# Performance work log

Hardware: AMD Instinct MI355X
Metric: run time of the kernel (lower is better)

Reference implementation:

```python
import jax, jax.numpy as jnp
import numpy as np

T = 4096
C = 2048
N_FEAT = 2048
NEG = -1e30  # finite stand-in for -inf so fully-masked (padding) rows stay NaN-free


def setup_inputs() -> dict:
    key = jax.random.key(0)
    kx, kw, kb = jax.random.split(key, 3)
    x = jax.random.normal(kx, (T, C), dtype=jnp.float32)
    # Dense(features=3*n_feat): kernel (C, 3*n_feat), bias (3*n_feat,)
    W = jax.random.normal(kw, (C, 3 * N_FEAT), dtype=jnp.float32) * (1.0 / np.sqrt(C))
    b = jax.random.normal(kb, (3 * N_FEAT,), dtype=jnp.float32) * 0.01
    n_padd = 128
    return {"x": x, "W": W, "b": b, "n_padd": n_padd}


def reference(x, W, b, n_padd):
    T_, _ = x.shape
    qkv = x @ W + b                      # (T, 3*n_feat)
    q, k, v = jnp.split(qkv, 3, axis=1)  # each (T, n_feat)
    scale = 1.0 / jnp.sqrt(jnp.float32(q.shape[1]))
    att = (q @ k.T) * scale              # (T, T)
    rows = jnp.arange(T_)[:, None]
    cols = jnp.arange(T_)[None, :]
    # causal AND both row/col past the left padding
    mask = (cols <= rows) & (cols >= n_padd) & (rows >= n_padd)
    att = jnp.where(mask, att, NEG)
    p = jax.nn.softmax(att, axis=1)      # stable row softmax
    # kernel only stores rows >= n_padd; padding rows are zero
    p = jnp.where(rows >= n_padd, p, 0.0)
    y = p @ v                            # (T, n_feat)
    return y
```

## Files before the change

kernel.cpp:

```cpp
#include <hip/hip_runtime.h>
#include <cstdint>


#define T_DIM 4096
#define C_DIM 2048
#define NF    2048
#define N3    6144
#define NEGV  (-1e30f)

typedef __bf16 bf16x8 __attribute__((ext_vector_type(8)));
typedef __bf16 bf16x4 __attribute__((ext_vector_type(4)));
typedef float  f32x4  __attribute__((ext_vector_type(4)));

__device__ __forceinline__ void async_cp16(const void* g, void* l) {
    __builtin_amdgcn_global_load_lds(
        reinterpret_cast<const __attribute__((address_space(1))) unsigned int*>(
            reinterpret_cast<uintptr_t>(g)),
        reinterpret_cast<__attribute__((address_space(3))) unsigned int*>(
            reinterpret_cast<uintptr_t>(l)),
        16, 0, 0);
}

__device__ __forceinline__ void gemm_loop(const __bf16* A, const __bf16* B,
                                          int lda, int ldb, int m0, int n0,
                                          int kiters, __bf16* As, __bf16* Bs,
                                          f32x4 (&acc)[4][4]) {
    const int t    = threadIdx.x;
    const int wv   = t >> 6;
    const int lane = t & 63;
    const int srow = t >> 3;
    const int scol = (((t & 7) ^ (srow & 7)) << 3);
    const int wm   = (wv >> 1) << 6;
    const int wn   = (wv & 1) << 6;
    const int lrow = lane & 15;
    const int kq   = lane >> 4;
    const int swz  = lrow & 7;
    const int rc0  = ((kq ^ swz) << 3);
    const int rc1  = (((kq | 4) ^ swz) << 3);

    const __bf16* ga = A + (size_t)(m0 + srow) * lda + scol;
    const __bf16* gb = B + (size_t)(n0 + srow) * ldb + scol;

    for (int kk = 0; kk < kiters; ++kk) {
#pragma unroll
        for (int i = 0; i < 4; ++i) {
            async_cp16(ga + (size_t)(32 * i) * lda, &As[i * 2048 + wv * 512]);
            async_cp16(gb + (size_t)(32 * i) * ldb, &Bs[i * 2048 + wv * 512]);
        }
        ga += 64; gb += 64;
        __syncthreads();

#pragma unroll
        for (int kb = 0; kb < 2; ++kb) {
            const int rc = kb ? rc1 : rc0;
            bf16x8 af[4], bfr[4];
#pragma unroll
            for (int mi = 0; mi < 4; ++mi)
                af[mi] = *(const bf16x8*)&As[(wm + mi * 16 + lrow) * 64 + rc];
#pragma unroll
            for (int ni = 0; ni < 4; ++ni)
                bfr[ni] = *(const bf16x8*)&Bs[(wn + ni * 16 + lrow) * 64 + rc];
#pragma unroll
            for (int mi = 0; mi < 4; ++mi)
#pragma unroll
                for (int ni = 0; ni < 4; ++ni)
                    acc[mi][ni] = __builtin_amdgcn_mfma_f32_16x16x32_bf16(
                        af[mi], bfr[ni], acc[mi][ni], 0, 0, 0);
        }
        __syncthreads();
    }
}

__global__ void prep_kernel(const float* __restrict__ x,
                            __bf16* __restrict__ xb,
                            const float* __restrict__ W,
                            __bf16* __restrict__ Wt) {
    if (blockIdx.x < 2048) {
        const int n4 = (T_DIM * C_DIM) / 4;
        const int stride = 2048 * 256;
        for (int i = blockIdx.x * 256 + threadIdx.x; i < n4; i += stride) {
            float4 v = ((const float4*)x)[i];
            bf16x4 o;
            o[0] = (__bf16)v.x; o[1] = (__bf16)v.y;
            o[2] = (__bf16)v.z; o[3] = (__bf16)v.w;
            ((bf16x4*)xb)[i] = o;
        }
        return;
    }
    __shared__ float tile[32][33];
    const int tb = blockIdx.x - 2048;
    const int bx = (tb % (N3 / 32)) * 32;
    const int by = (tb / (N3 / 32)) * 32;
    const int tx = threadIdx.x & 31, ty = threadIdx.x >> 5;
#pragma unroll
    for (int i = 0; i < 32; i += 8)
        tile[ty + i][tx] = W[(size_t)(by + ty + i) * N3 + bx + tx];
    __syncthreads();
#pragma unroll
    for (int i = 0; i < 32; i += 8)
        Wt[(size_t)(bx + ty + i) * C_DIM + by + tx] = (__bf16)tile[tx][ty + i];
}

#define EPILOG_SETUP()                                     \
    const int t = threadIdx.x, wv = t >> 6, lane = t & 63; \
    const int wm = (wv >> 1) << 6, wn = (wv & 1) << 6;     \
    const int rq = (lane >> 4) << 2, cn = lane & 15

__global__ void __launch_bounds__(512)
qkv_gemm_kernel(const __bf16* __restrict__ xb, const __bf16* __restrict__ Wt,
                const float* __restrict__ bias, __bf16* __restrict__ qb,
                __bf16* __restrict__ kb, __bf16* __restrict__ vT) {
    __shared__ __bf16 As[3][256 * 64];
    __shared__ __bf16 Bs[3][128 * 64];

    const int t    = threadIdx.x;
    const int wv   = t >> 6;
    const int lane = t & 63;
    const int srow = t >> 3;
    const int scol = (((t & 7) ^ (srow & 7)) << 3);
    const int m0   = blockIdx.x * 256;
    const int n0   = blockIdx.y * 128;
    const int wmo  = (wv >> 1) << 6;
    const int wno  = (wv & 1) << 6;
    const int lrow = lane & 15;
    const int kq   = lane >> 4;
    const int swz  = lrow & 7;
    const int rc0  = ((kq ^ swz) << 3);
    const int rc1  = (((kq | 4) ^ swz) << 3);

    const __bf16* ga = xb + (size_t)(m0 + srow) * C_DIM + scol;
    const __bf16* gb = Wt + (size_t)(n0 + srow) * C_DIM + scol;

    f32x4 acc[4][4] = {};

    auto stage = [&](int kt, int s) {
        const __bf16* a  = ga + kt * 64;
        const __bf16* b2 = gb + kt * 64;
#pragma unroll
        for (int i = 0; i < 4; ++i)
            async_cp16(a + (size_t)(64 * i) * C_DIM, &As[s][i * 4096 + wv * 512]);
#pragma unroll
        for (int i = 0; i < 2; ++i)
            async_cp16(b2 + (size_t)(64 * i) * C_DIM, &Bs[s][i * 4096 + wv * 512]);
    };

    auto compute = [&](int s) {
        const __bf16* Ab = As[s];
        const __bf16* Bb = Bs[s];
        bf16x8 af[4][2], bfr[4][2];
#pragma unroll
        for (int mi = 0; mi < 4; ++mi) {
            const __bf16* r = &Ab[(wmo + mi * 16 + lrow) * 64];
            af[mi][0] = *(const bf16x8*)&r[rc0];
            af[mi][1] = *(const bf16x8*)&r[rc1];
        }
#pragma unroll
        for (int ni = 0; ni < 4; ++ni) {
            const __bf16* r = &Bb[(wno + ni * 16 + lrow) * 64];
            bfr[ni][0] = *(const bf16x8*)&r[rc0];
            bfr[ni][1] = *(const bf16x8*)&r[rc1];
        }
        __builtin_amdgcn_s_setprio(1);
#pragma unroll
        for (int kh = 0; kh < 2; ++kh)
#pragma unroll
            for (int mi = 0; mi < 4; ++mi)
#pragma unroll
                for (int ni = 0; ni < 4; ++ni)
                    acc[mi][ni] = __builtin_amdgcn_mfma_f32_16x16x32_bf16(
                        af[mi][kh], bfr[ni][kh], acc[mi][ni], 0, 0, 0);
        __builtin_amdgcn_s_setprio(0);
    };

    constexpr int KT = C_DIM / 64;
    stage(0, 0);
    stage(1, 1);

    int s0 = 0, s1 = 1, s2 = 2;
    for (int kt = 0; kt < KT - 2; ++kt) {
        asm volatile("s_waitcnt vmcnt(6)" ::: "memory");
        __builtin_amdgcn_s_barrier();
        asm volatile("" ::: "memory");
        stage(kt + 2, s2);
        compute(s0);
        int tmp = s0; s0 = s1; s1 = s2; s2 = tmp;
    }
    asm volatile("s_waitcnt vmcnt(6)" ::: "memory");
    __builtin_amdgcn_s_barrier();
    asm volatile("" ::: "memory");
    compute(s0);
    { int tmp = s0; s0 = s1; s1 = s2; s2 = tmp; }
    asm volatile("s_waitcnt vmcnt(0)" ::: "memory");
    __builtin_amdgcn_s_barrier();
    asm volatile("" ::: "memory");
    compute(s0);

    const int rq = (lane >> 4) << 2, cn = lane & 15;
    if (n0 >= 2 * NF) {
#pragma unroll
        for (int mi = 0; mi < 4; ++mi)
#pragma unroll
            for (int ni = 0; ni < 4; ++ni) {
                int col = n0 + wno + ni * 16 + cn;
                float bv = bias[col];
                bf16x4 o;
#pragma unroll
                for (int r = 0; r < 4; ++r) o[r] = (__bf16)(acc[mi][ni][r] + bv);
                int row = m0 + wmo + mi * 16 + rq;
                *(bf16x4*)&vT[(size_t)(col - 2 * NF) * T_DIM + row] = o;
            }
    } else {
#pragma unroll
        for (int mi = 0; mi < 4; ++mi)
#pragma unroll
            for (int ni = 0; ni < 4; ++ni) {
                int col = n0 + wno + ni * 16 + cn;
                float bv = bias[col];
#pragma unroll
                for (int r = 0; r < 4; ++r) {
                    int row = m0 + wmo + mi * 16 + rq + r;
                    float val = acc[mi][ni][r] + bv;
                    if (col < NF)
                        qb[(size_t)row * NF + col] = (__bf16)val;
                    else
                        kb[(size_t)row * NF + (col - NF)] = (__bf16)val;
                }
            }
    }
}

__global__ void __launch_bounds__(256)
sc_gemm_kernel(const __bf16* __restrict__ qb, const __bf16* __restrict__ kb,
               __bf16* __restrict__ S, const int* __restrict__ npadd_p) {
    int i = blockIdx.x;
    int mt = (int)((sqrtf(8.0f * (float)i + 1.0f) - 1.0f) * 0.5f);
    while ((mt + 1) * (mt + 2) / 2 <= i) ++mt;
    while (mt * (mt + 1) / 2 > i) --mt;
    int nt = i - mt * (mt + 1) / 2;
    const int m0 = mt * 128, n0 = nt * 128;
    const int npadd = *npadd_p;
    if (m0 + 128 <= npadd || n0 + 128 <= npadd) return;

    __shared__ __bf16 As[128 * 64];
    __shared__ __bf16 Bs[128 * 64];
    f32x4 acc[4][4] = {};
    gemm_loop(qb, kb, NF, NF, m0, n0, NF / 64, As, Bs, acc);

    const float scale = 0.022097086912079608f;
    EPILOG_SETUP();
#pragma unroll
    for (int mi = 0; mi < 4; ++mi)
#pragma unroll
        for (int ni = 0; ni < 4; ++ni) {
            int j = n0 + wn + ni * 16 + cn;
#pragma unroll
            for (int r = 0; r < 4; ++r) {
                int row = m0 + wm + mi * 16 + rq + r;
                S[(size_t)row * T_DIM + j] = (__bf16)(acc[mi][ni][r] * scale);
            }
        }
}

__global__ void __launch_bounds__(256)
softmax_kernel(const __bf16* __restrict__ S, __bf16* __restrict__ P,
               const int* __restrict__ npadd_p) {
    const int wv = threadIdx.x >> 6, lane = threadIdx.x & 63;
    const int row = blockIdx.x * 4 + wv;
    const int npadd = *npadd_p;
    __bf16* prow = P + (size_t)row * T_DIM;

    if (row < npadd) {
        bf16x8 z = {};
#pragma unroll
        for (int c = 0; c < 8; ++c) ((bf16x8*)prow)[c * 64 + lane] = z;
        return;
    }

    const __bf16* srow = S + (size_t)row * T_DIM;
    float vals[64];
    float mx = NEGV;
#pragma unroll
    for (int c = 0; c < 8; ++c) {
        if (c * 512 > row) {
#pragma unroll
            for (int e = 0; e < 8; ++e) vals[c * 8 + e] = NEGV;
            continue;
        }
        int j0 = c * 512 + lane * 8;
        bf16x8 v = ((const bf16x8*)srow)[c * 64 + lane];
#pragma unroll
        for (int e = 0; e < 8; ++e) {
            float f = (j0 + e >= npadd && j0 + e <= row) ? (float)v[e] : NEGV;
            vals[c * 8 + e] = f;
            mx = fmaxf(mx, f);
        }
    }
#pragma unroll
    for (int o = 32; o > 0; o >>= 1) mx = fmaxf(mx, __shfl_xor(mx, o));

    float sm = 0.f;
#pragma unroll
    for (int k = 0; k < 64; ++k) {
        vals[k] = exp2f((vals[k] - mx) * 1.4426950408889634f);
        sm += vals[k];
    }
#pragma unroll
    for (int o = 32; o > 0; o >>= 1) sm += __shfl_xor(sm, o);
    float inv = 1.0f / sm;

#pragma unroll
    for (int c = 0; c < 8; ++c) {
        bf16x8 o;
#pragma unroll
        for (int e = 0; e < 8; ++e) o[e] = (__bf16)(vals[c * 8 + e] * inv);
        ((bf16x8*)prow)[c * 64 + lane] = o;
    }
}

__global__ void __launch_bounds__(256)
pv_gemm_kernel(const __bf16* __restrict__ P, const __bf16* __restrict__ vT,
               float* __restrict__ out, const int* __restrict__ npadd_p) {
    const int idx = blockIdx.x;
    const int kskip = *npadd_p >> 6;
    int mt, nt, start, iters;
    bool atomic_out;
    if (idx < 256) {
        mt = idx & 15; nt = idx >> 4;
        int kt = (mt + 1) * 2 - kskip; if (kt < 0) kt = 0;
        start = kskip; iters = kt; atomic_out = false;
    } else {
        int j = idx - 256;
        mt = 16 + (j & 15); nt = (j >> 4) & 15;
        int half = j >> 8;
        int kt = (mt + 1) * 2 - kskip; if (kt < 0) kt = 0;
        int h0 = (kt + 1) >> 1;
        start = kskip + (half ? h0 : 0);
        iters = half ? kt - h0 : h0;
        atomic_out = true;
    }
    const int m0 = mt * 128, n0 = nt * 128;

    __shared__ __bf16 As[128 * 64];
    __shared__ __bf16 Bs[128 * 64];
    f32x4 acc[4][4] = {};
    gemm_loop(P + (size_t)start * 64, vT + (size_t)start * 64,
              T_DIM, T_DIM, m0, n0, iters, As, Bs, acc);

    EPILOG_SETUP();
#pragma unroll
    for (int mi = 0; mi < 4; ++mi)
#pragma unroll
        for (int ni = 0; ni < 4; ++ni) {
            int col = n0 + wn + ni * 16 + cn;
#pragma unroll
            for (int r = 0; r < 4; ++r) {
                int row = m0 + wm + mi * 16 + rq + r;
                float* p = &out[(size_t)row * NF + col];
                if (atomic_out) unsafeAtomicAdd(p, acc[mi][ni][r]);
                else            *p = acc[mi][ni][r];
            }
        }
}

extern "C" void kernel_launch(void* const* d_in, const int* in_sizes, int n_in,
                              void* d_out, int out_size, void* d_ws,
                              size_t ws_size, hipStream_t stream) {
    const float* x = (const float*)d_in[0];
    const float* W = (const float*)d_in[1];
    const float* b = (const float*)d_in[2];
    const int* npadd = (const int*)d_in[3];
    float* out = (float*)d_out;

    char* ws = (char*)d_ws;
    __bf16* xb = (__bf16*)(ws);
    __bf16* Wt = (__bf16*)(ws + (16ull << 20));
    __bf16* qb = (__bf16*)(ws + (40ull << 20));
    __bf16* kb = (__bf16*)(ws + (56ull << 20));
    __bf16* vT = (__bf16*)(ws + (72ull << 20));
    __bf16* S  = (__bf16*)(ws + (88ull << 20));
    __bf16* P  = (__bf16*)(ws + (40ull << 20));

    hipMemsetAsync(out + (size_t)2048 * NF, 0, (size_t)2048 * NF * 4, stream);

    prep_kernel<<<2048 + (N3 / 32) * (C_DIM / 32), 256, 0, stream>>>(x, xb, W, Wt);
    qkv_gemm_kernel<<<dim3(T_DIM / 256, N3 / 128), 512, 0, stream>>>(xb, Wt, b,
                                                                     qb, kb, vT);
    sc_gemm_kernel<<<528, 256, 0, stream>>>(qb, kb, S, npadd);
    softmax_kernel<<<T_DIM / 4, 256, 0, stream>>>(S, P, npadd);
    pv_gemm_kernel<<<768, 256, 0, stream>>>(P, vT, out, npadd);
}
```

Measured before the change: 335.4 us.

## Double-buffer shared GEMM loop and enlarge QKV GEMM tile to 256x384

```diff
diff --git a/kernel.cpp b/kernel.cpp
--- a/kernel.cpp
+++ b/kernel.cpp
@@ -25,6 +25,7 @@
                                           int lda, int ldb, int m0, int n0,
                                           int kiters, __bf16* As, __bf16* Bs,
                                           f32x4 (&acc)[4][4]) {
+    if (kiters <= 0) return;
     const int t    = threadIdx.x;
     const int wv   = t >> 6;
     const int lane = t & 63;
@@ -41,33 +42,51 @@
     const __bf16* ga = A + (size_t)(m0 + srow) * lda + scol;
     const __bf16* gb = B + (size_t)(n0 + srow) * ldb + scol;
 
+    auto stage = [&](int kk, int s) {
+#pragma unroll
+        for (int i = 0; i < 4; ++i) {
+            async_cp16(ga + kk * 64 + (size_t)(32 * i) * lda,
+                       &As[s * 8192 + i * 2048 + wv * 512]);
+            async_cp16(gb + kk * 64 + (size_t)(32 * i) * ldb,
+                       &Bs[s * 8192 + i * 2048 + wv * 512]);
+        }
+    };
+
+    stage(0, 0);
+    int buf = 0;
     for (int kk = 0; kk < kiters; ++kk) {
-#pragma unroll
-        for (int i = 0; i < 4; ++i) {
-            async_cp16(ga + (size_t)(32 * i) * lda, &As[i * 2048 + wv * 512]);
-            async_cp16(gb + (size_t)(32 * i) * ldb, &Bs[i * 2048 + wv * 512]);
-        }
-        ga += 64; gb += 64;
-        __syncthreads();
-
+        if (kk + 1 < kiters) {
+            stage(kk + 1, buf ^ 1);
+            asm volatile("s_waitcnt vmcnt(8)" ::: "memory");
+        } else {
+            asm volatile("s_waitcnt vmcnt(0)" ::: "memory");
+        }
+        __builtin_amdgcn_s_barrier();
+        asm volatile("" ::: "memory");
+        const __bf16* Ab = &As[buf * 8192];
+        const __bf16* Bb = &Bs[buf * 8192];
 #pragma unroll
         for (int kb = 0; kb < 2; ++kb) {
             const int rc = kb ? rc1 : rc0;
             bf16x8 af[4], bfr[4];
 #pragma unroll
             for (int mi = 0; mi < 4; ++mi)
-                af[mi] = *(const bf16x8*)&As[(wm + mi * 16 + lrow) * 64 + rc];
+                af[mi] = *(const bf16x8*)&Ab[(wm + mi * 16 + lrow) * 64 + rc];
 #pragma unroll
             for (int ni = 0; ni < 4; ++ni)
-                bfr[ni] = *(const bf16x8*)&Bs[(wn + ni * 16 + lrow) * 64 + rc];
+                bfr[ni] = *(const bf16x8*)&Bb[(wn + ni * 16 + lrow) * 64 + rc];
+            __builtin_amdgcn_s_setprio(1);
 #pragma unroll
             for (int mi = 0; mi < 4; ++mi)
 #pragma unroll
                 for (int ni = 0; ni < 4; ++ni)
                     acc[mi][ni] = __builtin_amdgcn_mfma_f32_16x16x32_bf16(
                         af[mi], bfr[ni], acc[mi][ni], 0, 0, 0);
-        }
-        __syncthreads();
+            __builtin_amdgcn_s_setprio(0);
+        }
+        asm volatile("" ::: "memory");
+        __builtin_amdgcn_s_barrier();
+        buf ^= 1;
     }
 }
 
@@ -110,8 +129,8 @@
 qkv_gemm_kernel(const __bf16* __restrict__ xb, const __bf16* __restrict__ Wt,
                 const float* __restrict__ bias, __bf16* __restrict__ qb,
                 __bf16* __restrict__ kb, __bf16* __restrict__ vT) {
-    __shared__ __bf16 As[3][256 * 64];
-    __shared__ __bf16 Bs[3][128 * 64];
+    __shared__ __bf16 As[2][256 * 64];
+    __shared__ __bf16 Bs[2][384 * 64];
 
     const int t    = threadIdx.x;
     const int wv   = t >> 6;
@@ -119,9 +138,9 @@
     const int srow = t >> 3;
     const int scol = (((t & 7) ^ (srow & 7)) << 3);
     const int m0   = blockIdx.x * 256;
-    const int n0   = blockIdx.y * 128;
-    const int wmo  = (wv >> 1) << 6;
-    const int wno  = (wv & 1) << 6;
+    const int n0   = blockIdx.y * 384;
+    const int wmo  = (wv >> 2) * 128;
+    const int wno  = (wv & 3) * 96;
     const int lrow = lane & 15;
     const int kq   = lane >> 4;
     const int swz  = lrow & 7;
@@ -131,7 +150,7 @@
     const __bf16* ga = xb + (size_t)(m0 + srow) * C_DIM + scol;
     const __bf16* gb = Wt + (size_t)(n0 + srow) * C_DIM + scol;
 
-    f32x4 acc[4][4] = {};
+    f32x4 acc[8][6] = {};
 
     auto stage = [&](int kt, int s) {
         const __bf16* a  = ga + kt * 64;
@@ -140,82 +159,61 @@
         for (int i = 0; i < 4; ++i)
             async_cp16(a + (size_t)(64 * i) * C_DIM, &As[s][i * 4096 + wv * 512]);
 #pragma unroll
-        for (int i = 0; i < 2; ++i)
+        for (int i = 0; i < 6; ++i)
             async_cp16(b2 + (size_t)(64 * i) * C_DIM, &Bs[s][i * 4096 + wv * 512]);
     };
 
-    auto compute = [&](int s) {
-        const __bf16* Ab = As[s];
-        const __bf16* Bb = Bs[s];
-        bf16x8 af[4][2], bfr[4][2];
-#pragma unroll
-        for (int mi = 0; mi < 4; ++mi) {
-            const __bf16* r = &Ab[(wmo + mi * 16 + lrow) * 64];
-            af[mi][0] = *(const bf16x8*)&r[rc0];
-            af[mi][1] = *(const bf16x8*)&r[rc1];
-        }
-#pragma unroll
-        for (int ni = 0; ni < 4; ++ni) {
-            const __bf16* r = &Bb[(wno + ni * 16 + lrow) * 64];
-            bfr[ni][0] = *(const bf16x8*)&r[rc0];
-            bfr[ni][1] = *(const bf16x8*)&r[rc1];
-        }
-        __builtin_amdgcn_s_setprio(1);
-#pragma unroll
-        for (int kh = 0; kh < 2; ++kh)
-#pragma unroll
-            for (int mi = 0; mi < 4; ++mi)
-#pragma unroll
-                for (int ni = 0; ni < 4; ++ni)
-                    acc[mi][ni] = __builtin_amdgcn_mfma_f32_16x16x32_bf16(
-                        af[mi][kh], bfr[ni][kh], acc[mi][ni], 0, 0, 0);
-        __builtin_amdgcn_s_setprio(0);
-    };
-
     constexpr int KT = C_DIM / 64;
     stage(0, 0);
-    stage(1, 1);
-
-    int s0 = 0, s1 = 1, s2 = 2;
-    for (int kt = 0; kt < KT - 2; ++kt) {
-        asm volatile("s_waitcnt vmcnt(6)" ::: "memory");
+    int buf = 0;
+    for (int kt = 0; kt < KT; ++kt) {
+        if (kt + 1 < KT) {
+            stage(kt + 1, buf ^ 1);
+            asm volatile("s_waitcnt vmcnt(10)" ::: "memory");
+        } else {
+            asm volatile("s_waitcnt vmcnt(0)" ::: "memory");
+        }
         __builtin_amdgcn_s_barrier();
         asm volatile("" ::: "memory");
-        stage(kt + 2, s2);
-        compute(s0);
-        int tmp = s0; s0 = s1; s1 = s2; s2 = tmp;
-    }
-    asm volatile("s_waitcnt vmcnt(6)" ::: "memory");
-    __builtin_amdgcn_s_barrier();
-    asm volatile("" ::: "memory");
-    compute(s0);
-    { int tmp = s0; s0 = s1; s1 = s2; s2 = tmp; }
-    asm volatile("s_waitcnt vmcnt(0)" ::: "memory");
-    __builtin_amdgcn_s_barrier();
-    asm volatile("" ::: "memory");
-    compute(s0);
+        const __bf16* Ab = As[buf];
+        const __bf16* Bb = Bs[buf];
+#pragma unroll
+        for (int kb2 = 0; kb2 < 2; ++kb2) {
+            const int rc = kb2 ? rc1 : rc0;
+            bf16x8 bfr[6];
+#pragma unroll
+            for (int ni = 0; ni < 6; ++ni)
+                bfr[ni] = *(const bf16x8*)&Bb[(wno + ni * 16 + lrow) * 64 + rc];
+            __builtin_amdgcn_s_setprio(1);
+#pragma unroll
+            for (int mi = 0; mi < 8; ++mi) {
+                bf16x8 af = *(const bf16x8*)&Ab[(wmo + mi * 16 + lrow) * 64 + rc];
+#pragma unroll
+                for (int ni = 0; ni < 6; ++ni)
+                    acc[mi][ni] = __builtin_amdgcn_mfma_f32_16x16x32_bf16(
+                        af, bfr[ni], acc[mi][ni], 0, 0, 0);
+            }
+            __builtin_amdgcn_s_setprio(0);
+        }
+        asm volatile("" ::: "memory");
+        __builtin_amdgcn_s_barrier();
+        buf ^= 1;
+    }
 
     const int rq = (lane >> 4) << 2, cn = lane & 15;
-    if (n0 >= 2 * NF) {
-#pragma unroll
-        for (int mi = 0; mi < 4; ++mi)
-#pragma unroll
-            for (int ni = 0; ni < 4; ++ni) {
-                int col = n0 + wno + ni * 16 + cn;
-                float bv = bias[col];
+#pragma unroll
+    for (int mi = 0; mi < 8; ++mi)
+#pragma unroll
+        for (int ni = 0; ni < 6; ++ni) {
+            int col = n0 + wno + ni * 16 + cn;
+            float bv = bias[col];
+            if (col >= 2 * NF) {
                 bf16x4 o;
 #pragma unroll
                 for (int r = 0; r < 4; ++r) o[r] = (__bf16)(acc[mi][ni][r] + bv);
                 int row = m0 + wmo + mi * 16 + rq;
                 *(bf16x4*)&vT[(size_t)(col - 2 * NF) * T_DIM + row] = o;
-            }
-    } else {
-#pragma unroll
-        for (int mi = 0; mi < 4; ++mi)
-#pragma unroll
-            for (int ni = 0; ni < 4; ++ni) {
-                int col = n0 + wno + ni * 16 + cn;
-                float bv = bias[col];
+            } else {
 #pragma unroll
                 for (int r = 0; r < 4; ++r) {
                     int row = m0 + wmo + mi * 16 + rq + r;
@@ -226,7 +224,7 @@
                         kb[(size_t)row * NF + (col - NF)] = (__bf16)val;
                 }
             }
-    }
+        }
 }
 
 __global__ void __launch_bounds__(256)
@@ -241,8 +239,8 @@
     const int npadd = *npadd_p;
     if (m0 + 128 <= npadd || n0 + 128 <= npadd) return;
 
-    __shared__ __bf16 As[128 * 64];
-    __shared__ __bf16 Bs[128 * 64];
+    __shared__ __bf16 As[2 * 128 * 64];
+    __shared__ __bf16 Bs[2 * 128 * 64];
     f32x4 acc[4][4] = {};
     gemm_loop(qb, kb, NF, NF, m0, n0, NF / 64, As, Bs, acc);
 
@@ -340,8 +338,8 @@
     }
     const int m0 = mt * 128, n0 = nt * 128;
 
-    __shared__ __bf16 As[128 * 64];
-    __shared__ __bf16 Bs[128 * 64];
+    __shared__ __bf16 As[2 * 128 * 64];
+    __shared__ __bf16 Bs[2 * 128 * 64];
     f32x4 acc[4][4] = {};
     gemm_loop(P + (size_t)start * 64, vT + (size_t)start * 64,
               T_DIM, T_DIM, m0, n0, iters, As, Bs, acc);
@@ -383,7 +381,7 @@
     hipMemsetAsync(out + (size_t)2048 * NF, 0, (size_t)2048 * NF * 4, stream);
 
     prep_kernel<<<2048 + (N3 / 32) * (C_DIM / 32), 256, 0, stream>>>(x, xb, W, Wt);
-    qkv_gemm_kernel<<<dim3(T_DIM / 256, N3 / 128), 512, 0, stream>>>(xb, Wt, b,
+    qkv_gemm_kernel<<<dim3(T_DIM / 256, N3 / 384), 512, 0, stream>>>(xb, Wt, b,
                                                                      qb, kb, vT);
     sc_gemm_kernel<<<528, 256, 0, stream>>>(qb, kb, S, npadd);
     softmax_kernel<<<T_DIM / 4, 256, 0, stream>>>(S, P, npadd);
```

Result: no change. 341.5 us (+1.8%).
